# Kernel tuning notes

Hardware: AMD Instinct MI355X
Metric: run time of the kernel (lower is better)

The kernel has to match this reference:

```python
import jax, jax.numpy as jnp
import numpy as np

N, E, IN, H, C = 50000, 1600000, 128, 64, 2
# calculate_theta2(d=2): Bernstein-beta polynomial coefficients (increasing power order)
THETAS = [[3.0, -3.0, 0.75], [0.0, 3.0, -1.5], [0.0, 0.0, 0.75]]
K = 3  # polynomial order d+1


def setup_inputs() -> dict:
    key = jax.random.key(0)
    ks = jax.random.split(key, 20)
    s = 0.05
    return {
        "in_feat": jax.random.normal(ks[0], (N, IN), jnp.float32),
        "src": jax.random.randint(ks[1], (E,), 0, N, jnp.int32),
        "dst": jax.random.randint(ks[2], (E,), 0, N, jnp.int32),
        "W1": jax.random.normal(ks[3], (IN, H), jnp.float32) * s,
        "b1": jnp.zeros((H,), jnp.float32),
        "W2": jax.random.normal(ks[4], (H, H), jnp.float32) * s,
        "b2": jnp.zeros((H,), jnp.float32),
        "Wres": jax.random.normal(ks[5], (H, H), jnp.float32) * s,
        "bres": jnp.zeros((H,), jnp.float32),
        "Wattn": jax.random.normal(ks[6], (H, 1), jnp.float32) * s,
        "battn": jnp.zeros((1,), jnp.float32),
        "Wf1": jax.random.normal(ks[7], (2 * H, H), jnp.float32) * s,
        "bf1": jnp.zeros((H,), jnp.float32),
        "Wf2": jax.random.normal(ks[8], (H, 1), jnp.float32) * s,
        "bf2": jnp.zeros((1,), jnp.float32),
        "W3": jax.random.normal(ks[9], (H, H), jnp.float32) * s,
        "b3": jnp.zeros((H,), jnp.float32),
        "W4": jax.random.normal(ks[10], (H, C), jnp.float32) * s,
        "b4": jnp.zeros((C,), jnp.float32),
    }


def reference(in_feat, src, dst, W1, b1, W2, b2, Wres, bres, Wattn, battn,
              Wf1, bf1, Wf2, bf2, W3, b3, W4, b4):
    relu = jax.nn.relu
    # degree normalization: in_degrees().clamp(min=1) ** -0.5
    deg = jax.ops.segment_sum(jnp.ones((E,), in_feat.dtype), dst, num_segments=N)
    d_invsqrt = jnp.clip(deg, 1.0, None) ** -0.5  # [N]
    d_invsqrt = d_invsqrt[:, None]

    def spmm(x):  # update_all(copy_u, sum): aggregate over incoming edges
        return jax.ops.segment_sum(x[src], dst, num_segments=N)

    def laplacian(x):  # x - D^{-1/2} A D^{-1/2} x
        return x - spmm(x * d_invsqrt) * d_invsqrt

    # MLP preprocessing (dropout = identity in eval mode)
    h_pre = relu(in_feat @ W1 + b1)
    h_pre = relu(h_pre @ W2 + b2)
    res = h_pre @ Wres + bres

    # Laplacian power basis shared across branches (same math as per-branch loops)
    feats = [h_pre]
    for _ in range(K - 1):
        feats.append(laplacian(feats[-1]))

    branch_outputs = [sum(th[k] * feats[k] for k in range(K)) for th in THETAS]
    h_stack = jnp.stack(branch_outputs, axis=1)  # [N, B, H]

    # attention fusion over branches
    attn_scores = (h_stack @ Wattn + battn)[..., 0]       # [N, B]
    attn_weights = jax.nn.softmax(attn_scores, axis=1)[..., None]
    attn_fused = jnp.sum(h_stack * attn_weights, axis=1)  # [N, H]
    mean_fused = jnp.mean(h_stack, axis=1)                # [N, H]

    fusion_input = jnp.concatenate([attn_fused, mean_fused], axis=-1)  # [N, 2H]
    fusion_weight = jax.nn.sigmoid(relu(fusion_input @ Wf1 + bf1) @ Wf2 + bf2)  # [N, 1]

    fused = 0.1 * fusion_weight * attn_fused + (1.0 - fusion_weight) * mean_fused
    fused = fused + 0.8 * res
    fused = relu(fused @ W3 + b3)
    logits = fused @ W4 + b4
    return logits
```

## Files before the change

### kernel.cpp

```cpp
#include <hip/hip_runtime.h>
#include <hip/hip_fp16.h>
#include <math.h>


#define BSHIFT 7
#define BNODES 128
#define BMAX   512
#define EPT    32
#define CHUNK  (256 * EPT)
#define CAP    8192
#define F8SCALE 8.0f
#define F8INV  0.125f

typedef _Float16 h2v __attribute__((ext_vector_type(2)));
typedef float f2v __attribute__((ext_vector_type(2)));

__device__ __forceinline__ h2v as_h2(unsigned int u) {
    union { unsigned int u; h2v h; } c; c.u = u; return c.h;
}

__device__ __forceinline__ void fma4(float4& acc, float s, const float4 w) {
    acc.x += s * w.x; acc.y += s * w.y; acc.z += s * w.z; acc.w += s * w.w;
}

__device__ __forceinline__ float2 pack_half4(float x, float y, float z, float w) {
    union { __half2 h[2]; float2 f; } u;
    u.h[0] = __floats2half2_rn(x, y);
    u.h[1] = __floats2half2_rn(z, w);
    return u.f;
}

__device__ __forceinline__ void acch4(float4& a, float2 p) {
    union { float2 f; __half2 h[2]; } u; u.f = p;
    float2 lo = __half22float2(u.h[0]);
    float2 hi = __half22float2(u.h[1]);
    a.x += lo.x; a.y += lo.y; a.z += hi.x; a.w += hi.y;
}

__device__ __forceinline__ void accq(float4& a, float2 pA, float2 pB,
                                     float2 pC, float2 pD) {
    union { float2 f; __half2 h[2]; } A, B, C, D;
    A.f = pA; B.f = pB; C.f = pC; D.f = pD;
    __half2 s0 = __hadd2(__hadd2(A.h[0], B.h[0]), __hadd2(C.h[0], D.h[0]));
    __half2 s1 = __hadd2(__hadd2(A.h[1], B.h[1]), __hadd2(C.h[1], D.h[1]));
    float2 lo = __half22float2(s0), hi = __half22float2(s1);
    a.x += lo.x; a.y += lo.y; a.z += hi.x; a.w += hi.y;
}

__device__ __forceinline__ void accd(float4& a, float2 pA, float2 pB) {
    union { float2 f; __half2 h[2]; } A, B;
    A.f = pA; B.f = pB;
    __half2 s0 = __hadd2(A.h[0], B.h[0]);
    __half2 s1 = __hadd2(A.h[1], B.h[1]);
    float2 lo = __half22float2(s0), hi = __half22float2(s1);
    a.x += lo.x; a.y += lo.y; a.z += hi.x; a.w += hi.y;
}

__device__ __forceinline__ void accf8(float4& a, unsigned int v) {
    f2v lo = __builtin_amdgcn_cvt_pk_f32_fp8(v, false);
    f2v hi = __builtin_amdgcn_cvt_pk_f32_fp8(v, true);
    a.x += lo[0]; a.y += lo[1]; a.z += hi[0]; a.w += hi[1];
}


__global__ __launch_bounds__(256) void fused1_k(const int* __restrict__ dst,
                                                int* __restrict__ bucketCount,
                                                int E, int B,
                                                const float* __restrict__ Xg,
                                                const float* __restrict__ W1,
                                                const float* __restrict__ b1,
                                                float* __restrict__ h1, int N,
                                                const float* __restrict__ Wf1,
                                                const float* __restrict__ W3,
                                                unsigned int* __restrict__ Wf1h,
                                                unsigned int* __restrict__ W3h,
                                                int eb, int d1b) {
    __shared__ float smem[256 * 36];
    int bid = blockIdx.x;
    if (bid < eb) {
        int* cnt = (int*)smem;
        for (int i = threadIdx.x; i < B; i += 256) cnt[i] = 0;
        __syncthreads();
        int base = bid * CHUNK;
        #pragma unroll
        for (int t = 0; t < EPT; t++) {
            int e = base + t * 256 + threadIdx.x;
            if (e < E) atomicAdd(&cnt[dst[e] >> BSHIFT], 1);
        }
        __syncthreads();
        for (int i = threadIdx.x; i < B; i += 256)
            if (cnt[i] > 0) atomicAdd(&bucketCount[i], cnt[i]);
        return;
    }
    bid -= eb;
    if (bid < d1b) {
        int n0 = bid * 256;
        int n = n0 + threadIdx.x;
        bool act = (n < N);
        const float4* W = (const float4*)W1;
        const float4* Bb = (const float4*)b1;
        float4 acc[16];
        #pragma unroll
        for (int j = 0; j < 16; j++) acc[j] = Bb[j];
        if (act) {
            const float4* X = (const float4*)Xg + (size_t)n * 32;
            float4 a = X[0];
            #pragma unroll 1
            for (int kc = 0; kc < 32; kc++) {
                float4 an = a;
                if (kc + 1 < 32) an = X[kc + 1];
                const float4* wrow = W + kc * 64;
                #pragma unroll
                for (int j = 0; j < 16; j++) {
                    fma4(acc[j], a.x, wrow[j]);
                    fma4(acc[j], a.y, wrow[16 + j]);
                    fma4(acc[j], a.z, wrow[32 + j]);
                    fma4(acc[j], a.w, wrow[48 + j]);
                }
                a = an;
            }
        }
        #pragma unroll
        for (int j = 0; j < 16; j++) {
            float4 v = acc[j];
            acc[j] = make_float4(fmaxf(v.x, 0.f), fmaxf(v.y, 0.f),
                                 fmaxf(v.z, 0.f), fmaxf(v.w, 0.f));
        }
        float4* o4 = (float4*)h1;
        #pragma unroll
        for (int r2 = 0; r2 < 2; r2++) {
            __syncthreads();
            float* myrow = &smem[threadIdx.x * 36];
            #pragma unroll
            for (int j = 0; j < 8; j++) *(float4*)&myrow[4 * j] = acc[r2 * 8 + j];
            __syncthreads();
            #pragma unroll
            for (int r = 0; r < 8; r++) {
                int idx = r * 256 + threadIdx.x;
                int row = idx >> 3, col = idx & 7;
                int gn = n0 + row;
                if (gn < N)
                    o4[(size_t)gn * 16 + r2 * 8 + col] =
                        *(float4*)&smem[row * 36 + col * 4];
            }
        }
        return;
    }
    bid -= d1b;
    int t = bid * 256 + threadIdx.x;
    if (t < 64 * 64) {
        int kk = t >> 6, j = t & 63;
        union { __half2 h; unsigned int u; } c;
        c.h = __floats2half2_rn(Wf1[(2 * kk) * 64 + j], Wf1[(2 * kk + 1) * 64 + j]);
        Wf1h[t] = c.u;
    } else if (t < 64 * 64 + 32 * 64) {
        int r = t - 64 * 64;
        int kk = r >> 6, j = r & 63;
        union { __half2 h; unsigned int u; } c;
        c.h = __floats2half2_rn(W3[(2 * kk) * 64 + j], W3[(2 * kk + 1) * 64 + j]);
        W3h[r] = c.u;
    }
}


__global__ __launch_bounds__(64) void bucket_scan_k(const int* __restrict__ bucketCount,
                                                    int* __restrict__ bucketPtr,
                                                    int* __restrict__ bucketCursor,
                                                    int* __restrict__ rowPtr,
                                                    int B, int N, int E) {
    int lane = threadIdx.x;
    const int PT = (BMAX + 63) / 64;
    int v[PT]; int s = 0;
    #pragma unroll
    for (int t = 0; t < PT; t++) {
        int i = lane * PT + t;
        v[t] = (i < B) ? bucketCount[i] : 0;
        s += v[t];
    }
    int x = s;
    #pragma unroll
    for (int off = 1; off < 64; off <<= 1) {
        int y = __shfl_up(x, off, 64);
        if (lane >= off) x += y;
    }
    int run = x - s;
    #pragma unroll
    for (int t = 0; t < PT; t++) {
        int i = lane * PT + t;
        if (i < B) { bucketPtr[i] = run; bucketCursor[i] = run; }
        run += v[t];
    }
    if (lane == 63) bucketPtr[B] = x;
    if (lane == 0) rowPtr[N] = E;
}


__global__ __launch_bounds__(256) void fused3_k(const int* __restrict__ src,
                                                const int* __restrict__ dst,
                                                int* __restrict__ bucketCursor,
                                                int* __restrict__ ebuf,
                                                int E, int B,
                                                const float* __restrict__ h1,
                                                const float* __restrict__ W2,
                                                const float* __restrict__ b2,
                                                const float* __restrict__ Wres,
                                                const float* __restrict__ bres,
                                                const float* __restrict__ Wattn,
                                                const float* __restrict__ dinv,
                                                float* __restrict__ hg,
                                                float2* __restrict__ hs2,
                                                float* __restrict__ resg,
                                                float* __restrict__ thv, int N,
                                                int eb, int d2b) {
    __shared__ float smem[256 * 36];
    int bid = blockIdx.x;
    if (bid < eb) {
        int* cnt = (int*)smem;
        int* base = cnt + BMAX;
        int* cur = base + BMAX;
        for (int i = threadIdx.x; i < B; i += 256) { cnt[i] = 0; cur[i] = 0; }
        __syncthreads();
        int cbase = bid * CHUNK;
        int d[EPT];
        #pragma unroll
        for (int t = 0; t < EPT; t++) {
            int e = cbase + t * 256 + threadIdx.x;
            d[t] = (e < E) ? dst[e] : -1;
            if (d[t] >= 0) atomicAdd(&cnt[d[t] >> BSHIFT], 1);
        }
        __syncthreads();
        for (int i = threadIdx.x; i < B; i += 256)
            if (cnt[i] > 0) base[i] = atomicAdd(&bucketCursor[i], cnt[i]);
        __syncthreads();
        #pragma unroll
        for (int t = 0; t < EPT; t++) {
            int e = cbase + t * 256 + threadIdx.x;
            if (d[t] >= 0) {
                int b = d[t] >> BSHIFT;
                int c = atomicAdd(&cur[b], 1);
                int pack = (src[e] & 0xFFFF) | ((d[t] & (BNODES - 1)) << 16);
                ebuf[base[b] + c] = pack;
            }
        }
        return;
    }
    bid -= eb;
    int n0 = bid * 256;
    int n = n0 + threadIdx.x;
    bool act = (n < N);
    const float4* W = (const float4*)W2;
    const float4* Bb = (const float4*)b2;
    float4 acc[16];
    #pragma unroll
    for (int j = 0; j < 16; j++) acc[j] = Bb[j];
    if (act) {
        const float4* X = (const float4*)h1 + (size_t)n * 16;
        float4 a = X[0];
        #pragma unroll 1
        for (int kc = 0; kc < 16; kc++) {
            float4 an = a;
            if (kc + 1 < 16) an = X[kc + 1];
            const float4* wrow = W + kc * 64;
            #pragma unroll
            for (int j = 0; j < 16; j++) {
                fma4(acc[j], a.x, wrow[j]);
                fma4(acc[j], a.y, wrow[16 + j]);
                fma4(acc[j], a.z, wrow[32 + j]);
                fma4(acc[j], a.w, wrow[48 + j]);
            }
            a = an;
        }
    }
    const float4* Wa = (const float4*)Wattn;
    float th = 0.f;
    #pragma unroll
    for (int j = 0; j < 16; j++) {
        float4 v = acc[j];
        v.x = fmaxf(v.x, 0.f); v.y = fmaxf(v.y, 0.f);
        v.z = fmaxf(v.z, 0.f); v.w = fmaxf(v.w, 0.f);
        acc[j] = v;
        float4 w = Wa[j];
        th += v.x * w.x + v.y * w.y + v.z * w.z + v.w * w.w;
    }
    if (act) thv[n] = th;
    float4* h4 = (float4*)hg;
    #pragma unroll
    for (int r2 = 0; r2 < 2; r2++) {
        __syncthreads();
        float* myrow = &smem[threadIdx.x * 36];
        #pragma unroll
        for (int j = 0; j < 8; j++) *(float4*)&myrow[4 * j] = acc[r2 * 8 + j];
        __syncthreads();
        #pragma unroll
        for (int r = 0; r < 8; r++) {
            int idx = r * 256 + threadIdx.x;
            int row = idx >> 3, col = idx & 7;
            int gn = n0 + row;
            if (gn < N) {
                float4 v = *(float4*)&smem[row * 36 + col * 4];
                h4[(size_t)gn * 16 + r2 * 8 + col] = v;
                float di = dinv[gn];
                hs2[(size_t)gn * 16 + r2 * 8 + col] =
                    pack_half4(v.x * di, v.y * di, v.z * di, v.w * di);
            }
        }
    }
    const float4* WR = (const float4*)Wres;
    const float4* BR = (const float4*)bres;
    float4 acc2[16];
    #pragma unroll
    for (int j = 0; j < 16; j++) acc2[j] = BR[j];
    #pragma unroll 1
    for (int kc = 0; kc < 16; kc++) {
        float4 a2 = acc[kc];
        const float4* wrow = WR + kc * 64;
        #pragma unroll
        for (int j = 0; j < 16; j++) {
            fma4(acc2[j], a2.x, wrow[j]);
            fma4(acc2[j], a2.y, wrow[16 + j]);
            fma4(acc2[j], a2.z, wrow[32 + j]);
            fma4(acc2[j], a2.w, wrow[48 + j]);
        }
    }
    float4* r4 = (float4*)resg;
    #pragma unroll
    for (int r2 = 0; r2 < 2; r2++) {
        __syncthreads();
        float* myrow = &smem[threadIdx.x * 36];
        #pragma unroll
        for (int j = 0; j < 8; j++) *(float4*)&myrow[4 * j] = acc2[r2 * 8 + j];
        __syncthreads();
        #pragma unroll
        for (int r = 0; r < 8; r++) {
            int idx = r * 256 + threadIdx.x;
            int row = idx >> 3, col = idx & 7;
            int gn = n0 + row;
            if (gn < N)
                r4[(size_t)gn * 16 + r2 * 8 + col] =
                    *(float4*)&smem[row * 36 + col * 4];
        }
    }
}


__global__ __launch_bounds__(256) void csr_build_k(const int* __restrict__ ebuf,
                                                   const int* __restrict__ bucketPtr,
                                                   int* __restrict__ rowPtr,
                                                   float* __restrict__ dinv,
                                                   int* __restrict__ srcSorted,
                                                   int N) {
    __shared__ int deg[BNODES];
    __shared__ int rp[BNODES + 1];
    __shared__ int cur[BNODES];
    __shared__ int stage[CAP];
    int b = blockIdx.x;
    int nodeBase = b << BSHIFT;
    int nNodes = min(BNODES, N - nodeBase);
    int eBase = bucketPtr[b];
    int eCnt = bucketPtr[b + 1] - eBase;
    for (int i = threadIdx.x; i < BNODES; i += 256) deg[i] = 0;
    __syncthreads();
    for (int i = threadIdx.x; i < eCnt; i += 256)
        atomicAdd(&deg[(ebuf[eBase + i] >> 16) & (BNODES - 1)], 1);
    __syncthreads();
    if (threadIdx.x < 64) {
        int lane = threadIdx.x;
        int d0 = deg[2 * lane], d1 = deg[2 * lane + 1];
        int s = d0 + d1;
        int x = s;
        #pragma unroll
        for (int off = 1; off < 64; off <<= 1) {
            int y = __shfl_up(x, off, 64);
            if (lane >= off) x += y;
        }
        int ex = x - s;
        rp[2 * lane] = ex;
        rp[2 * lane + 1] = ex + d0;
        cur[2 * lane] = ex;
        cur[2 * lane + 1] = ex + d0;
        if (lane == 63) rp[BNODES] = x;
    }
    __syncthreads();
    for (int j = threadIdx.x; j < nNodes; j += 256) {
        rowPtr[nodeBase + j] = eBase + rp[j];
        int dg = deg[j];
        dinv[nodeBase + j] = rsqrtf((float)(dg > 1 ? dg : 1));
    }
    if (eCnt <= CAP) {
        for (int i = threadIdx.x; i < eCnt; i += 256) {
            int p = ebuf[eBase + i];
            int ld = (p >> 16) & (BNODES - 1);
            int pos = atomicAdd(&cur[ld], 1);
            stage[pos] = p & 0xFFFF;
        }
        __syncthreads();
        for (int i = threadIdx.x; i < eCnt; i += 256)
            srcSorted[eBase + i] = stage[i];
    } else {
        for (int i = threadIdx.x; i < eCnt; i += 256) {
            int p = ebuf[eBase + i];
            int ld = (p >> 16) & (BNODES - 1);
            int pos = atomicAdd(&cur[ld], 1);
            srcSorted[eBase + pos] = p & 0xFFFF;
        }
    }
}


__global__ __launch_bounds__(256) void spmm_k(const float2* __restrict__ xs,
                                              const int* __restrict__ srcs,
                                              const int* __restrict__ rowPtr,
                                              const float* __restrict__ dinv,
                                              const float* __restrict__ Wattn,
                                              float4* __restrict__ u,
                                              unsigned int* __restrict__ us,
                                              float* __restrict__ tav, int N) {
    int node = (blockIdx.x * 256 + threadIdx.x) >> 6;
    if (node >= N) return;
    int lane = threadIdx.x & 63;
    int sub = lane >> 4;
    int q = lane & 15;
    int s0 = rowPtr[node], s1 = rowPtr[node + 1];
    float4 a0 = make_float4(0.f, 0.f, 0.f, 0.f);
    int i = s0 + sub;
    if (i + 12 < s1) {
        int cA = srcs[i], cB = srcs[i + 4], cC = srcs[i + 8], cD = srcs[i + 12];
        i += 16;
        for (; i + 12 < s1; i += 16) {
            int nA = srcs[i], nB = srcs[i + 4], nC = srcs[i + 8], nD = srcs[i + 12];
            float2 vA = xs[(size_t)cA * 16 + q];
            float2 vB = xs[(size_t)cB * 16 + q];
            float2 vC = xs[(size_t)cC * 16 + q];
            float2 vD = xs[(size_t)cD * 16 + q];
            accq(a0, vA, vB, vC, vD);
            cA = nA; cB = nB; cC = nC; cD = nD;
        }
        float2 vA = xs[(size_t)cA * 16 + q];
        float2 vB = xs[(size_t)cB * 16 + q];
        float2 vC = xs[(size_t)cC * 16 + q];
        float2 vD = xs[(size_t)cD * 16 + q];
        accq(a0, vA, vB, vC, vD);
    }
    for (; i + 4 < s1; i += 8) {
        int sA = srcs[i];
        int sB = srcs[i + 4];
        float2 vA = xs[(size_t)sA * 16 + q];
        float2 vB = xs[(size_t)sB * 16 + q];
        accd(a0, vA, vB);
    }
    if (i < s1) {
        float2 vA = xs[(size_t)srcs[i] * 16 + q];
        acch4(a0, vA);
    }
    #pragma unroll
    for (int m = 16; m < 64; m <<= 1) {
        a0.x += __shfl_xor(a0.x, m, 64);
        a0.y += __shfl_xor(a0.y, m, 64);
        a0.z += __shfl_xor(a0.z, m, 64);
        a0.w += __shfl_xor(a0.w, m, 64);
    }
    if (sub == 0) {
        float di = dinv[node];
        float4 r = make_float4(a0.x * di, a0.y * di, a0.z * di, a0.w * di);
        u[(size_t)node * 16 + q] = r;
        float sc = di * F8SCALE;
        unsigned int pk = 0;
        pk = __builtin_amdgcn_cvt_pk_fp8_f32(r.x * sc, r.y * sc, pk, false);
        pk = __builtin_amdgcn_cvt_pk_fp8_f32(r.z * sc, r.w * sc, pk, true);
        us[(size_t)node * 16 + q] = pk;
        float4 w = ((const float4*)Wattn)[q];
        float p = r.x * w.x + r.y * w.y + r.z * w.z + r.w * w.w;
        #pragma unroll
        for (int m = 1; m < 16; m <<= 1) p += __shfl_xor(p, m, 64);
        if (lane == 0) tav[node] = p;
    }
}


#define TL_PAD 68
#define BS_HPAD 136

__global__ __launch_bounds__(256) void tail_k(const unsigned int* __restrict__ u1s,
                                              const int* __restrict__ srcs,
                                              const int* __restrict__ rowPtr,
                                              const float* __restrict__ dinv,
                                              const float* __restrict__ hg,
                                              const float* __restrict__ u1g,
                                              const float* __restrict__ resg,
                                              const float* __restrict__ thv,
                                              const float* __restrict__ tav,
                                              const float* __restrict__ Wattn,
                                              const float* __restrict__ battn,
                                              const unsigned int* __restrict__ Wf1h,
                                              const float* __restrict__ bf1,
                                              const float* __restrict__ Wf2,
                                              const float* __restrict__ bf2,
                                              const unsigned int* __restrict__ W3h,
                                              const float* __restrict__ b3,
                                              const float* __restrict__ W4,
                                              const float* __restrict__ b4,
                                              float2* __restrict__ out, int N) {
    __shared__ float lds[4 * TL_PAD];
    __shared__ _Float16 bsl[4 * BS_HPAD];
    int w = threadIdx.x >> 6;
    int lane = threadIdx.x & 63;
    int node = blockIdx.x * 4 + w;
    if (node >= N) return;
    int sub = lane >> 4, q = lane & 15;
    float hj = hg[(size_t)node * 64 + lane];
    float u1j = u1g[(size_t)node * 64 + lane];
    float resj = resg[(size_t)node * 64 + lane];
    float th = thv[node], ta = tav[node], ba = battn[0];
    float waj = Wattn[lane];
    float dinv_n = dinv[node] * F8INV;
    {
        int s0 = rowPtr[node], s1 = rowPtr[node + 1];
        float4 a0 = make_float4(0.f, 0.f, 0.f, 0.f);
        float4 a1 = a0;
        int i = s0 + sub;
        if (i + 12 < s1) {
            int cA = srcs[i], cB = srcs[i + 4], cC = srcs[i + 8], cD = srcs[i + 12];
            i += 16;
            for (; i + 12 < s1; i += 16) {
                int nA = srcs[i], nB = srcs[i + 4], nC = srcs[i + 8], nD = srcs[i + 12];
                unsigned int vA = u1s[(size_t)cA * 16 + q];
                unsigned int vB = u1s[(size_t)cB * 16 + q];
                unsigned int vC = u1s[(size_t)cC * 16 + q];
                unsigned int vD = u1s[(size_t)cD * 16 + q];
                accf8(a0, vA); accf8(a1, vB); accf8(a0, vC); accf8(a1, vD);
                cA = nA; cB = nB; cC = nC; cD = nD;
            }
            unsigned int vA = u1s[(size_t)cA * 16 + q];
            unsigned int vB = u1s[(size_t)cB * 16 + q];
            unsigned int vC = u1s[(size_t)cC * 16 + q];
            unsigned int vD = u1s[(size_t)cD * 16 + q];
            accf8(a0, vA); accf8(a1, vB); accf8(a0, vC); accf8(a1, vD);
        }
        for (; i + 4 < s1; i += 8) {
            unsigned int vA = u1s[(size_t)srcs[i] * 16 + q];
            unsigned int vB = u1s[(size_t)srcs[i + 4] * 16 + q];
            accf8(a0, vA); accf8(a1, vB);
        }
        if (i < s1) {
            unsigned int vA = u1s[(size_t)srcs[i] * 16 + q];
            accf8(a0, vA);
        }
        a0.x += a1.x; a0.y += a1.y; a0.z += a1.z; a0.w += a1.w;
        #pragma unroll
        for (int m = 16; m < 64; m <<= 1) {
            a0.x += __shfl_xor(a0.x, m, 64);
            a0.y += __shfl_xor(a0.y, m, 64);
            a0.z += __shfl_xor(a0.z, m, 64);
            a0.w += __shfl_xor(a0.w, m, 64);
        }
        if (sub == 0) {
            *(float4*)&lds[w * TL_PAD + q * 4] =
                make_float4(a0.x * dinv_n, a0.y * dinv_n,
                            a0.z * dinv_n, a0.w * dinv_n);
        }
    }
    float u2j = lds[w * TL_PAD + lane];
    float tb = u2j * waj;
    #pragma unroll
    for (int m = 1; m < 64; m <<= 1) tb += __shfl_xor(tb, m, 64);
    float s0 = 0.75f * th + 1.5f * ta + 0.75f * tb + ba;
    float s1 = 1.5f * th - 1.5f * tb + ba;
    float s2 = 0.75f * th - 1.5f * ta + 0.75f * tb + ba;
    float mx = fmaxf(s0, fmaxf(s1, s2));
    float e0 = expf(s0 - mx), e1 = expf(s1 - mx), e2 = expf(s2 - mx);
    float inv = 1.f / (e0 + e1 + e2);
    float w0 = e0 * inv, w1 = e1 * inv, w2 = e2 * inv;
    float ca = 0.75f * w0 + 1.5f * w1 + 0.75f * w2;
    float cb = 1.5f * (w0 - w2);
    float cc = 0.75f * w0 - 1.5f * w1 + 0.75f * w2;
    float afj = ca * hj + cb * u1j + cc * u2j;
    _Float16* bsh = &bsl[w * BS_HPAD];
    bsh[lane] = (_Float16)afj;
    bsh[64 + lane] = (_Float16)hj;
    float t0 = bf1[lane], t1 = 0.f, t2 = 0.f, t3 = 0.f;
    #pragma unroll 1
    for (int kk = 0; kk < 64; kk += 4) {
        uint4 br = *(const uint4*)&bsh[2 * kk];
        unsigned int w0_ = Wf1h[(kk + 0) * 64 + lane];
        unsigned int w1_ = Wf1h[(kk + 1) * 64 + lane];
        unsigned int w2_ = Wf1h[(kk + 2) * 64 + lane];
        unsigned int w3_ = Wf1h[(kk + 3) * 64 + lane];
        t0 = __builtin_amdgcn_fdot2(as_h2(br.x), as_h2(w0_), t0, false);
        t1 = __builtin_amdgcn_fdot2(as_h2(br.y), as_h2(w1_), t1, false);
        t2 = __builtin_amdgcn_fdot2(as_h2(br.z), as_h2(w2_), t2, false);
        t3 = __builtin_amdgcn_fdot2(as_h2(br.w), as_h2(w3_), t3, false);
    }
    float t = fmaxf((t0 + t1) + (t2 + t3), 0.f);
    float fwacc = t * Wf2[lane];
    #pragma unroll
    for (int m = 1; m < 64; m <<= 1) fwacc += __shfl_xor(fwacc, m, 64);
    float fw = 1.f / (1.f + expf(-(fwacc + bf2[0])));
    float fj = 0.1f * fw * afj + (1.f - fw) * hj + 0.8f * resj;
    bsh[lane] = (_Float16)fj;
    float g0 = b3[lane], g1 = 0.f, g2 = 0.f, g3 = 0.f;
    #pragma unroll 1
    for (int kk = 0; kk < 32; kk += 4) {
        uint4 br = *(const uint4*)&bsh[2 * kk];
        unsigned int w0_ = W3h[(kk + 0) * 64 + lane];
        unsigned int w1_ = W3h[(kk + 1) * 64 + lane];
        unsigned int w2_ = W3h[(kk + 2) * 64 + lane];
        unsigned int w3_ = W3h[(kk + 3) * 64 + lane];
        g0 = __builtin_amdgcn_fdot2(as_h2(br.x), as_h2(w0_), g0, false);
        g1 = __builtin_amdgcn_fdot2(as_h2(br.y), as_h2(w1_), g1, false);
        g2 = __builtin_amdgcn_fdot2(as_h2(br.z), as_h2(w2_), g2, false);
        g3 = __builtin_amdgcn_fdot2(as_h2(br.w), as_h2(w3_), g3, false);
    }
    float g = fmaxf((g0 + g1) + (g2 + g3), 0.f);
    float2 w4 = ((const float2*)W4)[lane];
    float l0 = g * w4.x, l1 = g * w4.y;
    #pragma unroll
    for (int m = 1; m < 64; m <<= 1) {
        l0 += __shfl_xor(l0, m, 64);
        l1 += __shfl_xor(l1, m, 64);
    }
    if (lane == 0) out[node] = make_float2(l0 + b4[0], l1 + b4[1]);
}


extern "C" void kernel_launch(void* const* d_in, const int* in_sizes, int n_in,
                              void* d_out, int out_size, void* d_ws, size_t ws_size,
                              hipStream_t stream) {
    const float* in_feat = (const float*)d_in[0];
    const int*   src     = (const int*)d_in[1];
    const int*   dst     = (const int*)d_in[2];
    const float* W1   = (const float*)d_in[3];
    const float* b1   = (const float*)d_in[4];
    const float* W2   = (const float*)d_in[5];
    const float* b2   = (const float*)d_in[6];
    const float* Wres = (const float*)d_in[7];
    const float* bres = (const float*)d_in[8];
    const float* Wattn = (const float*)d_in[9];
    const float* battn = (const float*)d_in[10];
    const float* Wf1  = (const float*)d_in[11];
    const float* bf1  = (const float*)d_in[12];
    const float* Wf2  = (const float*)d_in[13];
    const float* bf2  = (const float*)d_in[14];
    const float* W3   = (const float*)d_in[15];
    const float* b3   = (const float*)d_in[16];
    const float* W4   = (const float*)d_in[17];
    const float* b4   = (const float*)d_in[18];

    const int N = in_sizes[0] / 128;
    const int E = in_sizes[1];
    const int B = (N + BNODES - 1) >> BSHIFT;

    char* p = (char*)d_ws;
    auto take = [&](size_t bytes) -> char* {
        char* r = p;
        p += (bytes + 255) & ~(size_t)255;
        return r;
    };
    int*   bucketCount  = (int*)take((size_t)(B + 1) * 4);
    int*   bucketPtr    = (int*)take((size_t)(B + 1) * 4);
    int*   bucketCursor = (int*)take((size_t)(B + 1) * 4);
    int*   rowPtr       = (int*)take((size_t)(N + 1) * 4);
    float* dinv         = (float*)take((size_t)N * 4);
    int*   srcSorted    = (int*)take((size_t)E * 4);
    int*   ebuf         = (int*)take((size_t)E * 4);
    float* thv          = (float*)take((size_t)N * 4);
    float* tav          = (float*)take((size_t)N * 4);
    unsigned int* Wf1h  = (unsigned int*)take((size_t)64 * 64 * 4);
    unsigned int* W3h   = (unsigned int*)take((size_t)32 * 64 * 4);
    float* h1  = (float*)take((size_t)N * 256);
    float* h   = (float*)take((size_t)N * 256);
    float* hs  = (float*)take((size_t)N * 128);
    float* res = (float*)take((size_t)N * 256);
    float* u1  = (float*)take((size_t)N * 256);
    unsigned int* u1s = (unsigned int*)take((size_t)N * 64);

    int eb = (E + CHUNK - 1) / CHUNK;
    int dqb = (N + 255) / 256;
    int spb = (N * 64 + 255) / 256;
    int tlb = (N + 3) / 4;

    hipMemsetAsync(bucketCount, 0, (size_t)B * 4, stream);

    fused1_k<<<eb + dqb + 24, 256, 0, stream>>>(dst, bucketCount, E, B,
                                                in_feat, W1, b1, h1, N,
                                                Wf1, W3, Wf1h, W3h, eb, dqb);
    bucket_scan_k<<<1, 64, 0, stream>>>(bucketCount, bucketPtr, bucketCursor,
                                        rowPtr, B, N, E);
    fused3_k<<<eb + dqb, 256, 0, stream>>>(src, dst, bucketCursor, ebuf, E, B,
                                           h1, W2, b2, Wres, bres, Wattn, dinv,
                                           h, (float2*)hs, res, thv, N, eb, dqb);

    csr_build_k<<<B, 256, 0, stream>>>(ebuf, bucketPtr, rowPtr, dinv, srcSorted, N);

    spmm_k<<<spb, 256, 0, stream>>>((const float2*)hs, srcSorted, rowPtr, dinv,
                                    Wattn, (float4*)u1, u1s, tav, N);

    tail_k<<<tlb, 256, 0, stream>>>(u1s, srcSorted, rowPtr, dinv,
                                    h, u1, res, thv, tav, Wattn, battn,
                                    Wf1h, bf1, Wf2, bf2, W3h, b3, W4, b4,
                                    (float2*)d_out, N);
}
```

Measured before the change: 329.7 us.

## Fuse dense MLP stage with dinv computation and use fp16 dot-product matmuls

Per-node degrees are now counted with global atomics in the first kernel, so dinv is computed in a combined scan kernel before fused3 rather than in csr_build. That lets fused3 write the dinv-scaled fp16 features directly. The W2 and Wres matmuls are rewritten as one wavefront per node, using packed fp16 weights and fdot2, with no register-heavy per-thread row loop or LDS transpose. The cost is an extra global atomic per edge, a memset of the degree array, and lower-precision weights in these layers.

```diff
diff --git a/kernel.cpp b/kernel.cpp
--- a/kernel.cpp
+++ b/kernel.cpp
@@ -62,9 +62,18 @@
     a.x += lo[0]; a.y += lo[1]; a.z += hi[0]; a.w += hi[1];
 }
 
+__device__ __forceinline__ void pack_pair(const float* __restrict__ W,
+                                          unsigned int* __restrict__ Wh, int r) {
+    int kk = r >> 6, j = r & 63;
+    union { __half2 h; unsigned int u; } c;
+    c.h = __floats2half2_rn(W[(2 * kk) * 64 + j], W[(2 * kk + 1) * 64 + j]);
+    Wh[r] = c.u;
+}
+
 
 __global__ __launch_bounds__(256) void fused1_k(const int* __restrict__ dst,
                                                 int* __restrict__ bucketCount,
+                                                int* __restrict__ degN,
                                                 int E, int B,
                                                 const float* __restrict__ Xg,
                                                 const float* __restrict__ W1,
@@ -72,8 +81,12 @@
                                                 float* __restrict__ h1, int N,
                                                 const float* __restrict__ Wf1,
                                                 const float* __restrict__ W3,
+                                                const float* __restrict__ W2,
+                                                const float* __restrict__ Wres,
                                                 unsigned int* __restrict__ Wf1h,
                                                 unsigned int* __restrict__ W3h,
+                                                unsigned int* __restrict__ W2h,
+                                                unsigned int* __restrict__ Wresh,
                                                 int eb, int d1b) {
     __shared__ float smem[256 * 36];
     int bid = blockIdx.x;
@@ -85,7 +98,11 @@
         #pragma unroll
         for (int t = 0; t < EPT; t++) {
             int e = base + t * 256 + threadIdx.x;
-            if (e < E) atomicAdd(&cnt[dst[e] >> BSHIFT], 1);
+            if (e < E) {
+                int d = dst[e];
+                atomicAdd(&cnt[d >> BSHIFT], 1);
+                atomicAdd(&degN[d], 1);
+            }
         }
         __syncthreads();
         for (int i = threadIdx.x; i < B; i += 256)
@@ -148,52 +165,57 @@
     }
     bid -= d1b;
     int t = bid * 256 + threadIdx.x;
-    if (t < 64 * 64) {
-        int kk = t >> 6, j = t & 63;
-        union { __half2 h; unsigned int u; } c;
-        c.h = __floats2half2_rn(Wf1[(2 * kk) * 64 + j], Wf1[(2 * kk + 1) * 64 + j]);
-        Wf1h[t] = c.u;
-    } else if (t < 64 * 64 + 32 * 64) {
-        int r = t - 64 * 64;
-        int kk = r >> 6, j = r & 63;
-        union { __half2 h; unsigned int u; } c;
-        c.h = __floats2half2_rn(W3[(2 * kk) * 64 + j], W3[(2 * kk + 1) * 64 + j]);
-        W3h[r] = c.u;
-    }
-}
-
-
-__global__ __launch_bounds__(64) void bucket_scan_k(const int* __restrict__ bucketCount,
-                                                    int* __restrict__ bucketPtr,
-                                                    int* __restrict__ bucketCursor,
-                                                    int* __restrict__ rowPtr,
-                                                    int B, int N, int E) {
-    int lane = threadIdx.x;
-    const int PT = (BMAX + 63) / 64;
-    int v[PT]; int s = 0;
-    #pragma unroll
-    for (int t = 0; t < PT; t++) {
-        int i = lane * PT + t;
-        v[t] = (i < B) ? bucketCount[i] : 0;
-        s += v[t];
-    }
-    int x = s;
-    #pragma unroll
-    for (int off = 1; off < 64; off <<= 1) {
-        int y = __shfl_up(x, off, 64);
-        if (lane >= off) x += y;
-    }
-    int run = x - s;
-    #pragma unroll
-    for (int t = 0; t < PT; t++) {
-        int i = lane * PT + t;
-        if (i < B) { bucketPtr[i] = run; bucketCursor[i] = run; }
-        run += v[t];
-    }
-    if (lane == 63) bucketPtr[B] = x;
-    if (lane == 0) rowPtr[N] = E;
-}
-
+    if (t < 4096) pack_pair(Wf1, Wf1h, t);
+    else if (t < 6144) pack_pair(W3, W3h, t - 4096);
+    else if (t < 8192) pack_pair(W2, W2h, t - 6144);
+    else if (t < 10240) pack_pair(Wres, Wresh, t - 8192);
+}
+
+
+__global__ __launch_bounds__(256) void scan_dinv_k(const int* __restrict__ bucketCount,
+                                                   int* __restrict__ bucketPtr,
+                                                   int* __restrict__ bucketCursor,
+                                                   int* __restrict__ rowPtr,
+                                                   const int* __restrict__ degN,
+                                                   float* __restrict__ dinv,
+                                                   int B, int N, int E) {
+    if (blockIdx.x == 0) {
+        if (threadIdx.x >= 64) return;
+        int lane = threadIdx.x;
+        const int PT = (BMAX + 63) / 64;
+        int v[PT]; int s = 0;
+        #pragma unroll
+        for (int t = 0; t < PT; t++) {
+            int i = lane * PT + t;
+            v[t] = (i < B) ? bucketCount[i] : 0;
+            s += v[t];
+        }
+        int x = s;
+        #pragma unroll
+        for (int off = 1; off < 64; off <<= 1) {
+            int y = __shfl_up(x, off, 64);
+            if (lane >= off) x += y;
+        }
+        int run = x - s;
+        #pragma unroll
+        for (int t = 0; t < PT; t++) {
+            int i = lane * PT + t;
+            if (i < B) { bucketPtr[i] = run; bucketCursor[i] = run; }
+            run += v[t];
+        }
+        if (lane == 63) bucketPtr[B] = x;
+        if (lane == 0) rowPtr[N] = E;
+        return;
+    }
+    int n = (blockIdx.x - 1) * 256 + threadIdx.x;
+    if (n < N) {
+        int dg = degN[n];
+        dinv[n] = rsqrtf((float)(dg > 1 ? dg : 1));
+    }
+}
+
+
+#define D2_HPAD 72
 
 __global__ __launch_bounds__(256) void fused3_k(const int* __restrict__ src,
                                                 const int* __restrict__ dst,
@@ -201,24 +223,24 @@
                                                 int* __restrict__ ebuf,
                                                 int E, int B,
                                                 const float* __restrict__ h1,
-                                                const float* __restrict__ W2,
+                                                const unsigned int* __restrict__ W2h,
                                                 const float* __restrict__ b2,
-                                                const float* __restrict__ Wres,
+                                                const unsigned int* __restrict__ Wresh,
                                                 const float* __restrict__ bres,
                                                 const float* __restrict__ Wattn,
                                                 const float* __restrict__ dinv,
                                                 float* __restrict__ hg,
-                                                float2* __restrict__ hs2,
+                                                __half* __restrict__ hsh,
                                                 float* __restrict__ resg,
                                                 float* __restrict__ thv, int N,
-                                                int eb, int d2b) {
-    __shared__ float smem[256 * 36];
+                                                int eb) {
+    __shared__ int s_cnt[BMAX];
+    __shared__ int s_base[BMAX];
+    __shared__ int s_cur[BMAX];
+    __shared__ _Float16 bsl[4 * D2_HPAD];
     int bid = blockIdx.x;
     if (bid < eb) {
-        int* cnt = (int*)smem;
-        int* base = cnt + BMAX;
-        int* cur = base + BMAX;
-        for (int i = threadIdx.x; i < B; i += 256) { cnt[i] = 0; cur[i] = 0; }
+        for (int i = threadIdx.x; i < B; i += 256) { s_cnt[i] = 0; s_cur[i] = 0; }
         __syncthreads();
         int cbase = bid * CHUNK;
         int d[EPT];
@@ -226,127 +248,75 @@
         for (int t = 0; t < EPT; t++) {
             int e = cbase + t * 256 + threadIdx.x;
             d[t] = (e < E) ? dst[e] : -1;
-            if (d[t] >= 0) atomicAdd(&cnt[d[t] >> BSHIFT], 1);
+            if (d[t] >= 0) atomicAdd(&s_cnt[d[t] >> BSHIFT], 1);
         }
         __syncthreads();
         for (int i = threadIdx.x; i < B; i += 256)
-            if (cnt[i] > 0) base[i] = atomicAdd(&bucketCursor[i], cnt[i]);
+            if (s_cnt[i] > 0) s_base[i] = atomicAdd(&bucketCursor[i], s_cnt[i]);
         __syncthreads();
         #pragma unroll
         for (int t = 0; t < EPT; t++) {
             int e = cbase + t * 256 + threadIdx.x;
             if (d[t] >= 0) {
                 int b = d[t] >> BSHIFT;
-                int c = atomicAdd(&cur[b], 1);
+                int c = atomicAdd(&s_cur[b], 1);
                 int pack = (src[e] & 0xFFFF) | ((d[t] & (BNODES - 1)) << 16);
-                ebuf[base[b] + c] = pack;
+                ebuf[s_base[b] + c] = pack;
             }
         }
         return;
     }
     bid -= eb;
-    int n0 = bid * 256;
-    int n = n0 + threadIdx.x;
-    bool act = (n < N);
-    const float4* W = (const float4*)W2;
-    const float4* Bb = (const float4*)b2;
-    float4 acc[16];
+    int w = threadIdx.x >> 6;
+    int lane = threadIdx.x & 63;
+    int node = bid * 4 + w;
+    if (node >= N) return;
+    float h1j = h1[(size_t)node * 64 + lane];
+    float di = dinv[node];
+    float waj = Wattn[lane];
+    _Float16* bsh = &bsl[w * D2_HPAD];
+    bsh[lane] = (_Float16)h1j;
+    float t0 = b2[lane], t1 = 0.f, t2 = 0.f, t3 = 0.f;
+    #pragma unroll 1
+    for (int kk = 0; kk < 32; kk += 4) {
+        uint4 br = *(const uint4*)&bsh[2 * kk];
+        unsigned int w0_ = W2h[(kk + 0) * 64 + lane];
+        unsigned int w1_ = W2h[(kk + 1) * 64 + lane];
+        unsigned int w2_ = W2h[(kk + 2) * 64 + lane];
+        unsigned int w3_ = W2h[(kk + 3) * 64 + lane];
+        t0 = __builtin_amdgcn_fdot2(as_h2(br.x), as_h2(w0_), t0, false);
+        t1 = __builtin_amdgcn_fdot2(as_h2(br.y), as_h2(w1_), t1, false);
+        t2 = __builtin_amdgcn_fdot2(as_h2(br.z), as_h2(w2_), t2, false);
+        t3 = __builtin_amdgcn_fdot2(as_h2(br.w), as_h2(w3_), t3, false);
+    }
+    float hv = fmaxf((t0 + t1) + (t2 + t3), 0.f);
+    float th = hv * waj;
     #pragma unroll
-    for (int j = 0; j < 16; j++) acc[j] = Bb[j];
-    if (act) {
-        const float4* X = (const float4*)h1 + (size_t)n * 16;
-        float4 a = X[0];
-        #pragma unroll 1
-        for (int kc = 0; kc < 16; kc++) {
-            float4 an = a;
-            if (kc + 1 < 16) an = X[kc + 1];
-            const float4* wrow = W + kc * 64;
-            #pragma unroll
-            for (int j = 0; j < 16; j++) {
-                fma4(acc[j], a.x, wrow[j]);
-                fma4(acc[j], a.y, wrow[16 + j]);
-                fma4(acc[j], a.z, wrow[32 + j]);
-                fma4(acc[j], a.w, wrow[48 + j]);
-            }
-            a = an;
-        }
-    }
-    const float4* Wa = (const float4*)Wattn;
-    float th = 0.f;
-    #pragma unroll
-    for (int j = 0; j < 16; j++) {
-        float4 v = acc[j];
-        v.x = fmaxf(v.x, 0.f); v.y = fmaxf(v.y, 0.f);
-        v.z = fmaxf(v.z, 0.f); v.w = fmaxf(v.w, 0.f);
-        acc[j] = v;
-        float4 w = Wa[j];
-        th += v.x * w.x + v.y * w.y + v.z * w.z + v.w * w.w;
-    }
-    if (act) thv[n] = th;
-    float4* h4 = (float4*)hg;
-    #pragma unroll
-    for (int r2 = 0; r2 < 2; r2++) {
-        __syncthreads();
-        float* myrow = &smem[threadIdx.x * 36];
-        #pragma unroll
-        for (int j = 0; j < 8; j++) *(float4*)&myrow[4 * j] = acc[r2 * 8 + j];
-        __syncthreads();
-        #pragma unroll
-        for (int r = 0; r < 8; r++) {
-            int idx = r * 256 + threadIdx.x;
-            int row = idx >> 3, col = idx & 7;
-            int gn = n0 + row;
-            if (gn < N) {
-                float4 v = *(float4*)&smem[row * 36 + col * 4];
-                h4[(size_t)gn * 16 + r2 * 8 + col] = v;
-                float di = dinv[gn];
-                hs2[(size_t)gn * 16 + r2 * 8 + col] =
-                    pack_half4(v.x * di, v.y * di, v.z * di, v.w * di);
-            }
-        }
-    }
-    const float4* WR = (const float4*)Wres;
-    const float4* BR = (const float4*)bres;
-    float4 acc2[16];
-    #pragma unroll
-    for (int j = 0; j < 16; j++) acc2[j] = BR[j];
+    for (int m = 1; m < 64; m <<= 1) th += __shfl_xor(th, m, 64);
+    if (lane == 0) thv[node] = th;
+    hg[(size_t)node * 64 + lane] = hv;
+    hsh[(size_t)node * 64 + lane] = (__half)(hv * di);
+    bsh[lane] = (_Float16)hv;
+    float g0 = bres[lane], g1 = 0.f, g2 = 0.f, g3 = 0.f;
     #pragma unroll 1
-    for (int kc = 0; kc < 16; kc++) {
-        float4 a2 = acc[kc];
-        const float4* wrow = WR + kc * 64;
-        #pragma unroll
-        for (int j = 0; j < 16; j++) {
-            fma4(acc2[j], a2.x, wrow[j]);
-            fma4(acc2[j], a2.y, wrow[16 + j]);
-            fma4(acc2[j], a2.z, wrow[32 + j]);
-            fma4(acc2[j], a2.w, wrow[48 + j]);
-        }
-    }
-    float4* r4 = (float4*)resg;
-    #pragma unroll
-    for (int r2 = 0; r2 < 2; r2++) {
-        __syncthreads();
-        float* myrow = &smem[threadIdx.x * 36];
-        #pragma unroll
-        for (int j = 0; j < 8; j++) *(float4*)&myrow[4 * j] = acc2[r2 * 8 + j];
-        __syncthreads();
-        #pragma unroll
-        for (int r = 0; r < 8; r++) {
-            int idx = r * 256 + threadIdx.x;
-            int row = idx >> 3, col = idx & 7;
-            int gn = n0 + row;
-            if (gn < N)
-                r4[(size_t)gn * 16 + r2 * 8 + col] =
-                    *(float4*)&smem[row * 36 + col * 4];
-        }
-    }
+    for (int kk = 0; kk < 32; kk += 4) {
+        uint4 br = *(const uint4*)&bsh[2 * kk];
+        unsigned int w0_ = Wresh[(kk + 0) * 64 + lane];
+        unsigned int w1_ = Wresh[(kk + 1) * 64 + lane];
+        unsigned int w2_ = Wresh[(kk + 2) * 64 + lane];
+        unsigned int w3_ = Wresh[(kk + 3) * 64 + lane];
+        g0 = __builtin_amdgcn_fdot2(as_h2(br.x), as_h2(w0_), g0, false);
+        g1 = __builtin_amdgcn_fdot2(as_h2(br.y), as_h2(w1_), g1, false);
+        g2 = __builtin_amdgcn_fdot2(as_h2(br.z), as_h2(w2_), g2, false);
+        g3 = __builtin_amdgcn_fdot2(as_h2(br.w), as_h2(w3_), g3, false);
+    }
+    resg[(size_t)node * 64 + lane] = (g0 + g1) + (g2 + g3);
 }
 
 
 __global__ __launch_bounds__(256) void csr_build_k(const int* __restrict__ ebuf,
                                                    const int* __restrict__ bucketPtr,
                                                    int* __restrict__ rowPtr,
-                                                   float* __restrict__ dinv,
                                                    int* __restrict__ srcSorted,
                                                    int N) {
     __shared__ int deg[BNODES];
@@ -381,11 +351,8 @@
         if (lane == 63) rp[BNODES] = x;
     }
     __syncthreads();
-    for (int j = threadIdx.x; j < nNodes; j += 256) {
+    for (int j = threadIdx.x; j < nNodes; j += 256)
         rowPtr[nodeBase + j] = eBase + rp[j];
-        int dg = deg[j];
-        dinv[nodeBase + j] = rsqrtf((float)(dg > 1 ? dg : 1));
-    }
     if (eCnt <= CAP) {
         for (int i = threadIdx.x; i < eCnt; i += 256) {
             int p = ebuf[eBase + i];
@@ -659,13 +626,16 @@
     int*   bucketPtr    = (int*)take((size_t)(B + 1) * 4);
     int*   bucketCursor = (int*)take((size_t)(B + 1) * 4);
     int*   rowPtr       = (int*)take((size_t)(N + 1) * 4);
+    int*   degN         = (int*)take((size_t)N * 4);
     float* dinv         = (float*)take((size_t)N * 4);
     int*   srcSorted    = (int*)take((size_t)E * 4);
     int*   ebuf         = (int*)take((size_t)E * 4);
     float* thv          = (float*)take((size_t)N * 4);
     float* tav          = (float*)take((size_t)N * 4);
-    unsigned int* Wf1h  = (unsigned int*)take((size_t)64 * 64 * 4);
-    unsigned int* W3h   = (unsigned int*)take((size_t)32 * 64 * 4);
+    unsigned int* Wf1h  = (unsigned int*)take((size_t)4096 * 4);
+    unsigned int* W3h   = (unsigned int*)take((size_t)2048 * 4);
+    unsigned int* W2h   = (unsigned int*)take((size_t)2048 * 4);
+    unsigned int* Wresh = (unsigned int*)take((size_t)2048 * 4);
     float* h1  = (float*)take((size_t)N * 256);
     float* h   = (float*)take((size_t)N * 256);
     float* hs  = (float*)take((size_t)N * 128);
@@ -675,26 +645,29 @@
 
     int eb = (E + CHUNK - 1) / CHUNK;
     int dqb = (N + 255) / 256;
+    int wnb = (N + 3) / 4;
     int spb = (N * 64 + 255) / 256;
-    int tlb = (N + 3) / 4;
 
     hipMemsetAsync(bucketCount, 0, (size_t)B * 4, stream);
-
-    fused1_k<<<eb + dqb + 24, 256, 0, stream>>>(dst, bucketCount, E, B,
+    hipMemsetAsync(degN, 0, (size_t)N * 4, stream);
+
+    fused1_k<<<eb + dqb + 40, 256, 0, stream>>>(dst, bucketCount, degN, E, B,
                                                 in_feat, W1, b1, h1, N,
-                                                Wf1, W3, Wf1h, W3h, eb, dqb);
-    bucket_scan_k<<<1, 64, 0, stream>>>(bucketCount, bucketPtr, bucketCursor,
-                                        rowPtr, B, N, E);
-    fused3_k<<<eb + dqb, 256, 0, stream>>>(src, dst, bucketCursor, ebuf, E, B,
-                                           h1, W2, b2, Wres, bres, Wattn, dinv,
-                                           h, (float2*)hs, res, thv, N, eb, dqb);
-
-    csr_build_k<<<B, 256, 0, stream>>>(ebuf, bucketPtr, rowPtr, dinv, srcSorted, N);
+                                                Wf1, W3, W2, Wres,
+                                                Wf1h, W3h, W2h, Wresh, eb, dqb);
+    scan_dinv_k<<<1 + dqb, 256, 0, stream>>>(bucketCount, bucketPtr,
+                                             bucketCursor, rowPtr,
+                                             degN, dinv, B, N, E);
+    fused3_k<<<eb + wnb, 256, 0, stream>>>(src, dst, bucketCursor, ebuf, E, B,
+                                           h1, W2h, b2, Wresh, bres, Wattn,
+                                           dinv, h, (__half*)hs, res, thv, N, eb);
+
+    csr_build_k<<<B, 256, 0, stream>>>(ebuf, bucketPtr, rowPtr, srcSorted, N);
 
     spmm_k<<<spb, 256, 0, stream>>>((const float2*)hs, srcSorted, rowPtr, dinv,
                                     Wattn, (float4*)u1, u1s, tav, N);
 
-    tail_k<<<tlb, 256, 0, stream>>>(u1s, srcSorted, rowPtr, dinv,
+    tail_k<<<wnb, 256, 0, stream>>>(u1s, srcSorted, rowPtr, dinv,
                                     h, u1, res, thv, tav, Wattn, battn,
                                     Wf1h, bf1, Wf2, bf2, W3h, b3, W4, b4,
                                     (float2*)d_out, N);
```

Result: slower. 349.9 us (+6.1%).
